# Kernel tuning notes

Hardware: AMD Instinct MI355X
Metric: run time of the kernel (lower is better)

## Reference

```python
import jax, jax.numpy as jnp
import numpy as np
from jax import lax

B, T, D = 32, 1024, 512
UNITS, WINDOW = 512, 3


def setup_inputs() -> dict:
    key = jax.random.key(0)
    k1, k2 = jax.random.split(key)
    x = jax.random.normal(k1, (B, T, D), dtype=jnp.float32)
    kernel = jax.random.normal(k2, (WINDOW, D, UNITS * 3), dtype=jnp.float32) * 0.05
    return {"x": x, "kernel": kernel}


def reference(x, kernel):
    units = kernel.shape[2] // 3
    # valid conv1d, channels_last: [B, T, D] x [W, D, 3U] -> [B, T-W+1, 3U]
    conv = lax.conv_general_dilated(
        x, kernel, window_strides=(1,), padding='VALID',
        dimension_numbers=('NWC', 'WIO', 'NWC'))
    Z = conv[..., :units]
    F = conv[..., units:2 * units]
    O = conv[..., 2 * units:]
    z = jnp.tanh(Z)
    f = jax.nn.sigmoid(F)
    o = jax.nn.sigmoid(O)

    # fo-pooling recurrence over time (time-major scan)
    def step(c, zfo):
        z_t, f_t, o_t = zfo
        c_t = f_t * c + (1.0 - f_t) * z_t
        return c_t, o_t * c_t

    c0 = jnp.zeros((x.shape[0], units), dtype=x.dtype)
    zf = (z.transpose(1, 0, 2), f.transpose(1, 0, 2), o.transpose(1, 0, 2))
    _, hs = lax.scan(step, c0, zf)
    return hs.transpose(1, 0, 2)  # [B, T-W+1, units] (ret_sequence=True)
```

## Files before the change

### kernel.cpp

```cpp
#include <hip/hip_runtime.h>
#include <hip/hip_bf16.h>

typedef unsigned short u16;
typedef unsigned short u16x8 __attribute__((ext_vector_type(8)));
typedef short s16x8 __attribute__((ext_vector_type(8)));
typedef float f32x4 __attribute__((ext_vector_type(4)));

#define BATCH 32
#define TPAD 1024
#define TOUT 1022
#define DIM 512
#define KDIM 1536
#define NDIM 1536
#define MPAD (BATCH * TPAD)

#define XB_ELEMS  (MPAD * DIM + 1024)
#define XB_BYTES  (XB_ELEMS * 2)
#define WT_ELEMS  (NDIM * KDIM)
#define WT_BYTES  (WT_ELEMS * 2)
#define ACTS_OFF  (XB_BYTES + WT_BYTES)

__device__ __forceinline__ u16 f2bf(float f) {
    union { __hip_bfloat16 h; u16 u; } v;
    v.h = __float2bfloat16(f);
    return v.u;
}
__device__ __forceinline__ float bf2f(u16 u) {
    union { unsigned int i; float f; } v;
    v.i = ((unsigned int)u) << 16;
    return v.f;
}

__device__ __forceinline__ void gload_lds16(const void* g, void* l) {
    __builtin_amdgcn_global_load_lds(
        (const __attribute__((address_space(1))) void*)g,
        (__attribute__((address_space(3))) void*)l, 16, 0, 0);
}

#define BARRIER() do { asm volatile("" ::: "memory"); \
                       __builtin_amdgcn_s_barrier(); \
                       asm volatile("" ::: "memory"); } while (0)

__global__ __launch_bounds__(256) void cvt_x_kernel(const float* __restrict__ x,
                                                    u16* __restrict__ xb) {
    const int n = MPAD * DIM;
    const int ntot = XB_ELEMS;
    int i = (blockIdx.x * 256 + threadIdx.x) * 8;
    if (i >= ntot) return;
    if (i + 8 <= n) {
        const float4* p = (const float4*)(x + i);
        float4 a = p[0], b = p[1];
        u16x8 r;
        r[0] = f2bf(a.x); r[1] = f2bf(a.y); r[2] = f2bf(a.z); r[3] = f2bf(a.w);
        r[4] = f2bf(b.x); r[5] = f2bf(b.y); r[6] = f2bf(b.z); r[7] = f2bf(b.w);
        *(u16x8*)(xb + i) = r;
    } else {
        for (int q = 0; q < 8 && i + q < ntot; q++)
            xb[i + q] = (i + q < n) ? f2bf(x[i + q]) : (u16)0;
    }
}

__global__ __launch_bounds__(256) void cvt_w_kernel(const float* __restrict__ w,
                                                    u16* __restrict__ wT) {
    __shared__ u16 tile[32][33];
    int tx = threadIdx.x & 31, ty = threadIdx.x >> 5;
    int kt = blockIdx.x * 32, jt = blockIdx.y * 32;
#pragma unroll
    for (int q = 0; q < 4; q++) {
        int k = kt + ty + q * 8;
        tile[ty + q * 8][tx] = f2bf(w[(size_t)k * NDIM + jt + tx]);
    }
    __syncthreads();
#pragma unroll
    for (int q = 0; q < 4; q++) {
        int j = jt + ty + q * 8;
        wT[(size_t)j * KDIM + kt + tx] = tile[tx][ty + q * 8];
    }
}

__global__ __launch_bounds__(512, 2) void gemm_kernel(const u16* __restrict__ xb,
                                                      const u16* __restrict__ wT,
                                                      u16* __restrict__ acts) {
    __shared__ u16 lsA[256 * 64];
    __shared__ u16 lsB[256 * 64];

    const int tid  = threadIdx.x;
    const int lane = tid & 63;
    const int w    = tid >> 6;
    const int wr   = w >> 2;
    const int wc   = w & 3;

    const int wg  = blockIdx.x;
    const int gid = (wg & 7) * 96 + (wg >> 3);
    const int bm  = gid / 6;
    const int bn  = gid % 6;

    const int l15  = lane & 15;
    const int kgrp = (lane >> 4) * 16;
    const int xorv = (lane & 7) << 4;

    const int sc = ((lane & 7) ^ (lane >> 3)) << 4;
    const char* gsrc[8];
    char* ldst[8];
    {
        const char* gA = (const char*)xb;
        const char* gB = (const char*)wT;
#pragma unroll
        for (int g = 0; g < 4; g++) {
            int r0 = wr * 128 + g * 32 + wc * 8;
            int idx = (g < 2) ? g : (4 + g);
            gsrc[idx] = gA + (size_t)(bm * 256 + r0 + (lane >> 3)) * 1024 + sc;
            ldst[idx] = (char*)lsA + r0 * 128;
        }
#pragma unroll
        for (int h = 0; h < 4; h++) {
            int r0 = wc * 64 + h * 16 + wr * 8;
            int idx = 2 + h;
            gsrc[idx] = gB + (size_t)(bn * 256 + r0 + (lane >> 3)) * 3072 + sc;
            ldst[idx] = (char*)lsB + r0 * 128;
        }
    }

    f32x4 acc[8][4] = {};
    s16x8 a1[4][2];
    s16x8 a2[4][2];
    s16x8 b0[2][2];
    s16x8 b1v[2][2];

#define STAGE(IDX) gload_lds16(gsrc[IDX] + koff, ldst[IDX])

#define LOAD_A(DST, QM) \
    _Pragma("unroll") for (int ii = 0; ii < 4; ii++) \
    _Pragma("unroll") for (int kk = 0; kk < 2; kk++) { \
        int row = wr * 128 + (QM) * 64 + ii * 16 + l15; \
        int byte = (row * 128 + kk * 64 + kgrp) ^ xorv; \
        DST[ii][kk] = *(const s16x8*)((const char*)lsA + byte); }

#define LOAD_B(DST, QN) \
    _Pragma("unroll") for (int jj = 0; jj < 2; jj++) \
    _Pragma("unroll") for (int kk = 0; kk < 2; kk++) { \
        int row = wc * 64 + (QN) * 32 + jj * 16 + l15; \
        int byte = (row * 128 + kk * 64 + kgrp) ^ xorv; \
        DST[jj][kk] = *(const s16x8*)((const char*)lsB + byte); }

#define MFMA_QUAD(ASET, BSET, QM, QN) \
    __builtin_amdgcn_s_setprio(1); \
    _Pragma("unroll") for (int ii = 0; ii < 4; ii++) \
    _Pragma("unroll") for (int jj = 0; jj < 2; jj++) \
    _Pragma("unroll") for (int kk = 0; kk < 2; kk++) \
        acc[(QM)*4+ii][(QN)*2+jj] = __builtin_amdgcn_mfma_f32_16x16x32_bf16( \
            ASET[ii][kk], BSET[jj][kk], acc[(QM)*4+ii][(QN)*2+jj], 0, 0, 0); \
    __builtin_amdgcn_s_setprio(0);

    {
        size_t koff = 0;
        STAGE(0); STAGE(1); STAGE(2); STAGE(3);
        STAGE(4); STAGE(5); STAGE(6); STAGE(7);
    }
    asm volatile("s_waitcnt vmcnt(4)" ::: "memory");
    BARRIER();
    LOAD_A(a1, 0)
    LOAD_B(b0, 0)

    const int NT = KDIM / 64;
    for (int kt = 0; kt < NT; kt++) {
        const int knext = (kt + 1 == NT) ? 0 : (kt + 1);
        const size_t koff = (size_t)knext * 128;

        asm volatile("s_waitcnt vmcnt(2)" ::: "memory");
        BARRIER();
        MFMA_QUAD(a1, b0, 0, 0)
        LOAD_B(b1v, 1)

        asm volatile("s_waitcnt vmcnt(0)" ::: "memory");
        BARRIER();
        MFMA_QUAD(a1, b1v, 0, 1)
        LOAD_A(a2, 1)
        STAGE(0); STAGE(1); STAGE(2); STAGE(3);

        BARRIER();
        MFMA_QUAD(a2, b1v, 1, 1)
        STAGE(4); STAGE(5);

        asm volatile("s_waitcnt vmcnt(2)" ::: "memory");
        BARRIER();
        MFMA_QUAD(a2, b0, 1, 0)
        LOAD_A(a1, 0)
        LOAD_B(b0, 0)
        STAGE(6); STAGE(7);
    }

    asm volatile("s_waitcnt vmcnt(0)" ::: "memory");

#undef STAGE
#undef LOAD_A
#undef LOAD_B
#undef MFMA_QUAD

    const int m0 = bm * 256 + wr * 128 + ((lane >> 4) << 2);
    const int n0 = bn * 256 + wc * 64 + (lane & 15);
#pragma unroll
    for (int i = 0; i < 8; i++)
#pragma unroll
        for (int j = 0; j < 4; j++)
#pragma unroll
            for (int r = 0; r < 4; r++) {
                int m = m0 + i * 16 + r;
                int n = n0 + j * 16;
                acts[(size_t)m * NDIM + n] = f2bf(acc[i][j][r]);
            }
}

#define CHUNK 64
__global__ __launch_bounds__(1024) void scan_kernel(const u16* __restrict__ acts,
                                                    float* __restrict__ out) {
    __shared__ float sA[16][64];
    __shared__ float sB[16][64];
    const int lane = threadIdx.x & 63;
    const int w = threadIdx.x >> 6;
    const int b = blockIdx.x >> 3;
    const int u = ((blockIdx.x & 7) << 6) + lane;
    const u16* base = acts + (size_t)b * TPAD * NDIM;
    const int t0 = w * CHUNK;
    const int t1 = (t0 + CHUNK < TOUT) ? (t0 + CHUNK) : TOUT;

    float A = 1.f, Bc = 0.f;
    int t = t0;
    for (; t + 8 <= t1; t += 8) {
        u16 zv[8], fv[8];
#pragma unroll
        for (int q = 0; q < 8; q++) {
            const u16* r = base + (size_t)(t + q) * NDIM;
            zv[q] = r[u]; fv[q] = r[512 + u];
        }
#pragma unroll
        for (int q = 0; q < 8; q++) {
            float z = tanhf(bf2f(zv[q]));
            float f = 1.f / (1.f + __expf(-bf2f(fv[q])));
            Bc = f * Bc + (1.f - f) * z;
            A *= f;
        }
    }
    for (; t < t1; t++) {
        const u16* r = base + (size_t)t * NDIM;
        float z = tanhf(bf2f(r[u]));
        float f = 1.f / (1.f + __expf(-bf2f(r[512 + u])));
        Bc = f * Bc + (1.f - f) * z;
        A *= f;
    }
    sA[w][lane] = A; sB[w][lane] = Bc;
    __syncthreads();

    float c = 0.f;
    for (int w2 = 0; w2 < w; w2++)
        c = sA[w2][lane] * c + sB[w2][lane];

    float* ob = out + (size_t)b * (TOUT * DIM) + u;
    t = t0;
    for (; t + 8 <= t1; t += 8) {
        u16 zv[8], fv[8], ov[8];
#pragma unroll
        for (int q = 0; q < 8; q++) {
            const u16* r = base + (size_t)(t + q) * NDIM;
            zv[q] = r[u]; fv[q] = r[512 + u]; ov[q] = r[1024 + u];
        }
#pragma unroll
        for (int q = 0; q < 8; q++) {
            float z = tanhf(bf2f(zv[q]));
            float f = 1.f / (1.f + __expf(-bf2f(fv[q])));
            float o = 1.f / (1.f + __expf(-bf2f(ov[q])));
            c = f * c + (1.f - f) * z;
            ob[(size_t)(t + q) * DIM] = o * c;
        }
    }
    for (; t < t1; t++) {
        const u16* r = base + (size_t)t * NDIM;
        float z = tanhf(bf2f(r[u]));
        float f = 1.f / (1.f + __expf(-bf2f(r[512 + u])));
        float o = 1.f / (1.f + __expf(-bf2f(r[1024 + u])));
        c = f * c + (1.f - f) * z;
        ob[(size_t)t * DIM] = o * c;
    }
}

extern "C" void kernel_launch(void* const* d_in, const int* in_sizes, int n_in,
                              void* d_out, int out_size, void* d_ws, size_t ws_size,
                              hipStream_t stream) {
    const float* x = (const float*)d_in[0];
    const float* w = (const float*)d_in[1];
    float* out = (float*)d_out;
    char* ws = (char*)d_ws;

    u16* xb   = (u16*)ws;
    u16* wT   = (u16*)(ws + XB_BYTES);
    u16* acts = (u16*)(ws + ACTS_OFF);

    cvt_x_kernel<<<dim3((XB_ELEMS / 8 + 255) / 256), dim3(256), 0, stream>>>(x, xb);
    cvt_w_kernel<<<dim3(KDIM / 32, NDIM / 32), dim3(256), 0, stream>>>(w, wT);
    gemm_kernel<<<dim3(768), dim3(512), 0, stream>>>(xb, wT, acts);
    scan_kernel<<<dim3(256), dim3(1024), 0, stream>>>(acts, out);
}
```

Before: 221.7 us.

## Double-buffer LDS tiles in GEMM to prefetch two K-steps ahead

Splits the A and B shared-memory tiles into two buffers and has the main loop compute from one while global-to-LDS loads fill the other, prefetching two K-steps ahead. The vmcnt waits are re-tuned for the deeper queue of outstanding loads, and one barrier per iteration is removed. The aim is to hide global-load latency and cut the time MFMAs stall on barriers. In exchange, LDS use per block doubles to 128 KB, which likely allows only one 512-thread block per CU instead of two, despite the launch bounds.

```diff
diff --git a/kernel.cpp b/kernel.cpp
--- a/kernel.cpp
+++ b/kernel.cpp
@@ -81,8 +81,8 @@
 __global__ __launch_bounds__(512, 2) void gemm_kernel(const u16* __restrict__ xb,
                                                       const u16* __restrict__ wT,
                                                       u16* __restrict__ acts) {
-    __shared__ u16 lsA[256 * 64];
-    __shared__ u16 lsB[256 * 64];
+    __shared__ u16 lsA[2][256 * 64];
+    __shared__ u16 lsB[2][256 * 64];
 
     const int tid  = threadIdx.x;
     const int lane = tid & 63;
@@ -101,7 +101,7 @@
 
     const int sc = ((lane & 7) ^ (lane >> 3)) << 4;
     const char* gsrc[8];
-    char* ldst[8];
+    char* l0[8];
     {
         const char* gA = (const char*)xb;
         const char* gB = (const char*)wT;
@@ -110,14 +110,14 @@
             int r0 = wr * 128 + g * 32 + wc * 8;
             int idx = (g < 2) ? g : (4 + g);
             gsrc[idx] = gA + (size_t)(bm * 256 + r0 + (lane >> 3)) * 1024 + sc;
-            ldst[idx] = (char*)lsA + r0 * 128;
+            l0[idx] = (char*)lsA + r0 * 128;
         }
 #pragma unroll
         for (int h = 0; h < 4; h++) {
             int r0 = wc * 64 + h * 16 + wr * 8;
             int idx = 2 + h;
             gsrc[idx] = gB + (size_t)(bn * 256 + r0 + (lane >> 3)) * 3072 + sc;
-            ldst[idx] = (char*)lsB + r0 * 128;
+            l0[idx] = (char*)lsB + r0 * 128;
         }
     }
 
@@ -127,20 +127,20 @@
     s16x8 b0[2][2];
     s16x8 b1v[2][2];
 
-#define STAGE(IDX) gload_lds16(gsrc[IDX] + koff, ldst[IDX])
-
-#define LOAD_A(DST, QM) \
+#define STAGE(IDX) gload_lds16(gsrc[IDX] + koff, l0[IDX] + sbofs)
+
+#define LOAD_A(DST, QM, BUF) \
     _Pragma("unroll") for (int ii = 0; ii < 4; ii++) \
     _Pragma("unroll") for (int kk = 0; kk < 2; kk++) { \
         int row = wr * 128 + (QM) * 64 + ii * 16 + l15; \
-        int byte = (row * 128 + kk * 64 + kgrp) ^ xorv; \
+        int byte = ((row * 128 + kk * 64 + kgrp) ^ xorv) + (BUF) * 32768; \
         DST[ii][kk] = *(const s16x8*)((const char*)lsA + byte); }
 
-#define LOAD_B(DST, QN) \
+#define LOAD_B(DST, QN, BUF) \
     _Pragma("unroll") for (int jj = 0; jj < 2; jj++) \
     _Pragma("unroll") for (int kk = 0; kk < 2; kk++) { \
         int row = wc * 64 + (QN) * 32 + jj * 16 + l15; \
-        int byte = (row * 128 + kk * 64 + kgrp) ^ xorv; \
+        int byte = ((row * 128 + kk * 64 + kgrp) ^ xorv) + (BUF) * 32768; \
         DST[jj][kk] = *(const s16x8*)((const char*)lsB + byte); }
 
 #define MFMA_QUAD(ASET, BSET, QM, QN) \
@@ -153,41 +153,48 @@
     __builtin_amdgcn_s_setprio(0);
 
     {
-        size_t koff = 0;
+        size_t koff = 0, sbofs = 0;
         STAGE(0); STAGE(1); STAGE(2); STAGE(3);
         STAGE(4); STAGE(5); STAGE(6); STAGE(7);
     }
-    asm volatile("s_waitcnt vmcnt(4)" ::: "memory");
+    {
+        size_t koff = 128, sbofs = 32768;
+        STAGE(0); STAGE(1); STAGE(2); STAGE(3);
+        STAGE(4); STAGE(5); STAGE(6); STAGE(7);
+    }
+    asm volatile("s_waitcnt vmcnt(12)" ::: "memory");
     BARRIER();
-    LOAD_A(a1, 0)
-    LOAD_B(b0, 0)
+    LOAD_A(a1, 0, 0)
+    LOAD_B(b0, 0, 0)
 
     const int NT = KDIM / 64;
     for (int kt = 0; kt < NT; kt++) {
-        const int knext = (kt + 1 == NT) ? 0 : (kt + 1);
-        const size_t koff = (size_t)knext * 128;
-
-        asm volatile("s_waitcnt vmcnt(2)" ::: "memory");
+        const int c = kt & 1;
+        const int n = c ^ 1;
+
+        asm volatile("s_waitcnt vmcnt(10)" ::: "memory");
         BARRIER();
         MFMA_QUAD(a1, b0, 0, 0)
-        LOAD_B(b1v, 1)
-
-        asm volatile("s_waitcnt vmcnt(0)" ::: "memory");
+        LOAD_B(b1v, 1, c)
+
+        asm volatile("s_waitcnt vmcnt(8)" ::: "memory");
         BARRIER();
         MFMA_QUAD(a1, b1v, 0, 1)
-        LOAD_A(a2, 1)
-        STAGE(0); STAGE(1); STAGE(2); STAGE(3);
-
-        BARRIER();
+        LOAD_A(a2, 1, c)
+
         MFMA_QUAD(a2, b1v, 1, 1)
-        STAGE(4); STAGE(5);
-
-        asm volatile("s_waitcnt vmcnt(2)" ::: "memory");
+
+        asm volatile("s_waitcnt vmcnt(4)" ::: "memory");
         BARRIER();
         MFMA_QUAD(a2, b0, 1, 0)
-        LOAD_A(a1, 0)
-        LOAD_B(b0, 0)
-        STAGE(6); STAGE(7);
+        LOAD_A(a1, 0, n)
+        LOAD_B(b0, 0, n)
+        {
+            const size_t koff = (size_t)((kt + 2) % NT) * 128;
+            const size_t sbofs = (size_t)c * 32768;
+            STAGE(0); STAGE(1); STAGE(2); STAGE(3);
+            STAGE(4); STAGE(5); STAGE(6); STAGE(7);
+        }
     }
 
     asm volatile("s_waitcnt vmcnt(0)" ::: "memory");
```

Result: slower. 227.6 us (+2.7%).
